# Kernel tuning notes

Measured on AMD Instinct MI355X. Metric: run time of the kernel, lower is better.

## Reference

```python
import jax, jax.numpy as jnp
import numpy as np

GRID = 96  # grid_size from __init__


def setup_inputs() -> dict:
    key = jax.random.key(0)
    k1, k2 = jax.random.split(key)
    B, N, D = 8, 4096, 128
    node_features = jax.random.normal(k1, (N, D), dtype=jnp.float32)
    # pixel coordinates in [0, GRID)
    node_positions = jax.random.uniform(k2, (N, 2), dtype=jnp.float32) * GRID
    # sorted batch assignment with equal node counts per sample
    batch_idx = jnp.repeat(jnp.arange(B, dtype=jnp.int32), N // B)
    log_sigma = jnp.log(jnp.float32(4.0))  # learnable parameter, init sigma=4.0
    return {
        "node_features": node_features,
        "node_positions": node_positions,
        "batch_idx": batch_idx,
        "batch_size": B,
        "log_sigma": log_sigma,
    }


def reference(node_features, node_positions, batch_idx, batch_size, log_sigma):
    # node_features: (N, D); node_positions: (N, 2); batch_idx: (N,) sorted,
    # equal counts per sample (so grouping is a reshape).
    N, D = node_features.shape
    G = GRID
    coords = jnp.arange(G, dtype=jnp.float32)  # shared y and x coords
    dy = coords[None, :] - node_positions[:, 0:1]  # (N, G)
    dx = coords[None, :] - node_positions[:, 1:2]  # (N, G)
    # per-node distance map over the grid, matching torch's sqrt-then-square
    dist = jnp.sqrt(dy[:, :, None] ** 2 + dx[:, None, :] ** 2)  # (N, G, G)
    sigma = jnp.exp(log_sigma)
    w = jnp.exp(-(dist ** 2) / (2.0 * sigma ** 2)).reshape(N, G * G)
    w = w / (jnp.sum(w, axis=1, keepdims=True) + 1e-8)  # normalized splat weights
    n_per = N // batch_size
    f = node_features.reshape(batch_size, n_per, D)
    wB = w.reshape(batch_size, n_per, G * G)
    # grid[b, d, p] = sum_n f[b, n, d] * w[b, n, p]  (scatter-splat accumulation)
    grid = jnp.einsum('bnd,bnp->bdp', f, wB)
    return grid.reshape(batch_size, D, G, G)
```

## Files before the change

### kernel.cpp

```cpp
#include <hip/hip_runtime.h>
#include <hip/hip_bf16.h>

#define GG    96
#define DD    128
#define KC    32
#define APAD  40
#define RCUT  18
#define NWIN  18
#define NPER  512

typedef __attribute__((ext_vector_type(8))) short short8v;
typedef __attribute__((ext_vector_type(4))) float f32x4;

__global__ __launch_bounds__(256, 3) void splat_all(
    const float* __restrict__ f, const float* __restrict__ pos,
    const float* __restrict__ log_sigma, float* __restrict__ out,
    int Nn, int n_per)
{
    const int swz = ((int)blockIdx.x % 8) * GG + (int)blockIdx.x / 8;
    const int b = swz / GG;
    const int y = swz % GG;
    const int tid = (int)threadIdx.x;
    const int lane = tid & 63;
    const int wvid = tid >> 6;
    const int lr = lane & 15;
    const int kg = lane >> 4;
    const int kpw = tid & 15;
    const int nbase = b * NPER;
    const float yf = (float)y;

    __shared__ int ghist[8][GG];
    __shared__ int gpart[8][GG];
    __shared__ int spre[GG + 1];
    __shared__ int inv[NPER];
    __shared__ int wtot;
    __shared__ float spy_s[NPER], spx_s[NPER], sg_s[NPER];
    __shared__ float tSy[NPER], tSx[NPER];
    __shared__ __align__(16) unsigned short sW[2][GG][APAD];

    for (int i = tid; i < 8 * GG; i += 256) (&ghist[0][0])[i] = 0;
    __syncthreads();

    int binA, binB;
    {
        float pyA = pos[(size_t)(nbase + tid) * 2];
        float pyB = pos[(size_t)(nbase + tid + 256) * 2];
        binA = (int)floorf(pyA); binA = binA < 0 ? 0 : (binA > GG - 1 ? GG - 1 : binA);
        binB = (int)floorf(pyB); binB = binB < 0 ? 0 : (binB > GG - 1 ? GG - 1 : binB);
        atomicAdd(&ghist[wvid][binA], 1);
        atomicAdd(&ghist[4 + wvid][binB], 1);
    }
    const unsigned long long below = (lane == 0) ? 0ull : (~0ull >> (64 - lane));
    unsigned long long mA = ~0ull, mB = ~0ull;
#pragma unroll
    for (int bit = 0; bit < 7; ++bit) {
        unsigned long long bA = __ballot((binA >> bit) & 1);
        unsigned long long bB = __ballot((binB >> bit) & 1);
        mA &= ((binA >> bit) & 1) ? bA : ~bA;
        mB &= ((binB >> bit) & 1) ? bB : ~bB;
    }
    const int rA = __popcll(mA & below);
    const int rB = __popcll(mB & below);
    __syncthreads();

    int bc = 0;
    if (tid < GG) {
        int s = 0;
#pragma unroll
        for (int g = 0; g < 8; ++g) { gpart[g][tid] = s; s += ghist[g][tid]; }
        bc = s;
    }
    int xs = bc;
#pragma unroll
    for (int off = 1; off < 64; off <<= 1) {
        int v = __shfl_up(xs, off, 64);
        if (lane >= off) xs += v;
    }
    if (tid == 63) wtot = xs;
    __syncthreads();
    if (tid >= 64 && tid < GG) xs += wtot;
    if (tid < GG) spre[tid + 1] = xs;
    if (tid == 0) spre[0] = 0;
    __syncthreads();

    inv[spre[binA] + gpart[wvid][binA] + rA]     = tid;
    inv[spre[binB] + gpart[4 + wvid][binB] + rB] = tid + 256;
    __syncthreads();

    const int lob = y - RCUT < 0 ? 0 : y - RCUT;
    const int hib = y + RCUT > GG ? GG : y + RCUT;
    const int klo = spre[lob];
    const int khi = spre[hib];
    const int c0 = klo >> 5;
    const int c1 = (khi + 31) >> 5;
    const int jlo = c0 * KC, jhi = c1 * KC;
    const int nb = jhi - jlo;

    for (int i = tid; i < nb; i += 256) {
        int j = jlo + i, nl = inv[j];
        spy_s[j] = pos[(size_t)(nbase + nl) * 2 + 0];
        spx_s[j] = pos[(size_t)(nbase + nl) * 2 + 1];
    }
    __syncthreads();

    const float sig = expf(log_sigma[0]);
    const float inv2s2 = 1.0f / (2.0f * sig * sig);

    for (int i = tid; i < 2 * nb; i += 256) {
        int j = jlo + (i >> 1);
        float p = (i & 1) ? spx_s[j] : spy_s[j];
        int fp = (int)floorf(p);
        int w0 = fp - (NWIN - 1); if (w0 < 0) w0 = 0;
        int w1 = fp + NWIN;       if (w1 > GG - 1) w1 = GG - 1;
        float s = 0.f;
        for (int yy = w0; yy <= w1; ++yy) {
            float d = (float)yy - p;
            s += __expf(-d * d * inv2s2);
        }
        if (i & 1) tSx[j] = s; else tSy[j] = s;
    }
    __syncthreads();
    for (int i = tid; i < nb; i += 256) {
        int j = jlo + i;
        sg_s[j] = 1.0f / (tSy[j] * tSx[j] + 1e-8f);
    }
    __syncthreads();

    f32x4 acc[2][6];
#pragma unroll
    for (int mi = 0; mi < 2; ++mi)
#pragma unroll
        for (int ni = 0; ni < 6; ++ni) acc[mi][ni] = (f32x4){0.f, 0.f, 0.f, 0.f};

    const int ar0 = wvid * 32 + lr;
    const float* fcol = f + (size_t)nbase * DD + ar0;

#define WGEN(CC, BUF)                                                              \
    {                                                                              \
        const int j0_ = (CC) * KC + 2 * kpw;                                       \
        const float py0_ = spy_s[j0_], py1_ = spy_s[j0_ + 1];                      \
        const float px0_ = spx_s[j0_], px1_ = spx_s[j0_ + 1];                      \
        const float g0_ = sg_s[j0_],  g1_ = sg_s[j0_ + 1];                         \
        const float dy0_ = yf - py0_, dy1_ = yf - py1_;                            \
        const float ey0_ = __expf(-dy0_ * dy0_ * inv2s2) * g0_;                    \
        const float ey1_ = __expf(-dy1_ * dy1_ * inv2s2) * g1_;                    \
        _Pragma("unroll")                                                          \
        for (int i_ = 0; i_ < 6; ++i_) {                                           \
            int x_  = (tid + 256 * i_) >> 4;                                       \
            float xf_ = (float)x_;                                                 \
            float dx0_ = xf_ - px0_, dx1_ = xf_ - px1_;                            \
            float w0_ = ey0_ * __expf(-dx0_ * dx0_ * inv2s2);                      \
            float w1_ = ey1_ * __expf(-dx1_ * dx1_ * inv2s2);                      \
            __hip_bfloat162 bb_ = __float22bfloat162_rn(make_float2(w0_, w1_));    \
            *(unsigned int*)&sW[BUF][x_][2 * kpw] = *(unsigned int*)&bb_;          \
        }                                                                          \
    }

#define PKPAIR(X0, X1, HI, LO)                                                     \
    {                                                                              \
        __hip_bfloat162 h_ = __float22bfloat162_rn(make_float2((X0), (X1)));       \
        unsigned int hu_; __builtin_memcpy(&hu_, &h_, 4);                          \
        unsigned int b0_ = hu_ << 16, b1_ = hu_ & 0xFFFF0000u;                     \
        float h0_, h1_;                                                            \
        __builtin_memcpy(&h0_, &b0_, 4);                                           \
        __builtin_memcpy(&h1_, &b1_, 4);                                           \
        __hip_bfloat162 l_ = __float22bfloat162_rn(                                \
            make_float2((X0) - h0_, (X1) - h1_));                                  \
        (HI) = hu_; __builtin_memcpy(&(LO), &l_, 4);                               \
    }

    if (c0 < c1) WGEN(c0, 0);
    __syncthreads();

    int cur = 0;
    for (int c = c0; c < c1; ++c) {
        int4 iv0 = *(const int4*)&inv[c * KC + kg * 8];
        int4 iv1 = *(const int4*)&inv[c * KC + kg * 8 + 4];
        float v00 = fcol[(size_t)iv0.x * DD],      v01 = fcol[(size_t)iv0.y * DD];
        float v02 = fcol[(size_t)iv0.z * DD],      v03 = fcol[(size_t)iv0.w * DD];
        float v04 = fcol[(size_t)iv1.x * DD],      v05 = fcol[(size_t)iv1.y * DD];
        float v06 = fcol[(size_t)iv1.z * DD],      v07 = fcol[(size_t)iv1.w * DD];
        float v10 = fcol[(size_t)iv0.x * DD + 16], v11 = fcol[(size_t)iv0.y * DD + 16];
        float v12 = fcol[(size_t)iv0.z * DD + 16], v13 = fcol[(size_t)iv0.w * DD + 16];
        float v14 = fcol[(size_t)iv1.x * DD + 16], v15 = fcol[(size_t)iv1.y * DD + 16];
        float v16 = fcol[(size_t)iv1.z * DD + 16], v17 = fcol[(size_t)iv1.w * DD + 16];

        if (c + 1 < c1) WGEN(c + 1, cur ^ 1);

        union U { unsigned int u[4]; short8v v; } H0, L0, H1, L1;
        PKPAIR(v00, v01, H0.u[0], L0.u[0]);
        PKPAIR(v02, v03, H0.u[1], L0.u[1]);
        PKPAIR(v04, v05, H0.u[2], L0.u[2]);
        PKPAIR(v06, v07, H0.u[3], L0.u[3]);
        PKPAIR(v10, v11, H1.u[0], L1.u[0]);
        PKPAIR(v12, v13, H1.u[1], L1.u[1]);
        PKPAIR(v14, v15, H1.u[2], L1.u[2]);
        PKPAIR(v16, v17, H1.u[3], L1.u[3]);
        short8v cah0 = H0.v, cal0 = L0.v, cah1 = H1.v, cal1 = L1.v;

#pragma unroll
        for (int ni = 0; ni < 6; ++ni) {
            short8v bv = *(const short8v*)&sW[cur][ni * 16 + lr][kg * 8];
            acc[0][ni] = __builtin_amdgcn_mfma_f32_16x16x32_bf16(cah0, bv, acc[0][ni], 0, 0, 0);
            acc[1][ni] = __builtin_amdgcn_mfma_f32_16x16x32_bf16(cah1, bv, acc[1][ni], 0, 0, 0);
            acc[0][ni] = __builtin_amdgcn_mfma_f32_16x16x32_bf16(cal0, bv, acc[0][ni], 0, 0, 0);
            acc[1][ni] = __builtin_amdgcn_mfma_f32_16x16x32_bf16(cal1, bv, acc[1][ni], 0, 0, 0);
        }
        __syncthreads();
        cur ^= 1;
    }

#pragma unroll
    for (int mi = 0; mi < 2; ++mi)
#pragma unroll
        for (int ni = 0; ni < 6; ++ni) {
            const int d0 = wvid * 32 + mi * 16 + kg * 4;
            const int x  = ni * 16 + lr;
            float* op = out + (((size_t)b * DD + d0) * GG + y) * GG + x;
#pragma unroll
            for (int r = 0; r < 4; ++r)
                __builtin_nontemporal_store(acc[mi][ni][r], op + (size_t)r * GG * GG);
        }
#undef WGEN
#undef PKPAIR
}

extern "C" void kernel_launch(void* const* d_in, const int* in_sizes, int n_in,
                              void* d_out, int out_size, void* d_ws, size_t ws_size,
                              hipStream_t stream) {
    const float* feat = (const float*)d_in[0];
    const float* pos  = (const float*)d_in[1];
    const float* lsig = (const float*)d_in[4];

    const int N  = in_sizes[2];
    const int B  = out_size / (DD * GG * GG);
    const int n_per = N / B;

    splat_all<<<B * GG, 256, 0, stream>>>(feat, pos, lsig, (float*)d_out, N, n_per);
}
```

Before: 26.25 us.

## Drop bf16 low-part split of features and tighten chunk window alignment

Features were split into bf16 high and low parts with two MFMAs each. Now only the high part is kept, which halves the MFMA count and removes the residual packing work. The node-window chunking also starts at the exact first needed node instead of a 32-aligned boundary, clamped to the end of the sample, so fewer chunks are processed per row. Dropping the low part lowers feature precision to plain bf16, which risks accuracy-tolerance failures.

```diff
diff --git a/kernel.cpp b/kernel.cpp
--- a/kernel.cpp
+++ b/kernel.cpp
@@ -91,13 +91,13 @@
     const int hib = y + RCUT > GG ? GG : y + RCUT;
     const int klo = spre[lob];
     const int khi = spre[hib];
-    const int c0 = klo >> 5;
-    const int c1 = (khi + 31) >> 5;
-    const int jlo = c0 * KC, jhi = c1 * KC;
-    const int nb = jhi - jlo;
-
-    for (int i = tid; i < nb; i += 256) {
-        int j = jlo + i, nl = inv[j];
+    const int nch = (khi - klo + KC - 1) >> 5;
+    int j0 = klo;
+    if (j0 + nch * KC > NPER) j0 = NPER - nch * KC;
+    const int nbw = nch * KC;
+
+    for (int i = tid; i < nbw; i += 256) {
+        int j = j0 + i, nl = inv[j];
         spy_s[j] = pos[(size_t)(nbase + nl) * 2 + 0];
         spx_s[j] = pos[(size_t)(nbase + nl) * 2 + 1];
     }
@@ -106,8 +106,8 @@
     const float sig = expf(log_sigma[0]);
     const float inv2s2 = 1.0f / (2.0f * sig * sig);
 
-    for (int i = tid; i < 2 * nb; i += 256) {
-        int j = jlo + (i >> 1);
+    for (int i = tid; i < 2 * nbw; i += 256) {
+        int j = j0 + (i >> 1);
         float p = (i & 1) ? spx_s[j] : spy_s[j];
         int fp = (int)floorf(p);
         int w0 = fp - (NWIN - 1); if (w0 < 0) w0 = 0;
@@ -120,8 +120,8 @@
         if (i & 1) tSx[j] = s; else tSy[j] = s;
     }
     __syncthreads();
-    for (int i = tid; i < nb; i += 256) {
-        int j = jlo + i;
+    for (int i = tid; i < nbw; i += 256) {
+        int j = j0 + i;
         sg_s[j] = 1.0f / (tSy[j] * tSx[j] + 1e-8f);
     }
     __syncthreads();
@@ -137,7 +137,7 @@
 
 #define WGEN(CC, BUF)                                                              \
     {                                                                              \
-        const int j0_ = (CC) * KC + 2 * kpw;                                       \
+        const int j0_ = j0 + (CC) * KC + 2 * kpw;                                  \
         const float py0_ = spy_s[j0_], py1_ = spy_s[j0_ + 1];                      \
         const float px0_ = spx_s[j0_], px1_ = spx_s[j0_ + 1];                      \
         const float g0_ = sg_s[j0_],  g1_ = sg_s[j0_ + 1];                         \
@@ -156,26 +156,19 @@
         }                                                                          \
     }
 
-#define PKPAIR(X0, X1, HI, LO)                                                     \
+#define PKHI(X0, X1, HI)                                                           \
     {                                                                              \
         __hip_bfloat162 h_ = __float22bfloat162_rn(make_float2((X0), (X1)));       \
-        unsigned int hu_; __builtin_memcpy(&hu_, &h_, 4);                          \
-        unsigned int b0_ = hu_ << 16, b1_ = hu_ & 0xFFFF0000u;                     \
-        float h0_, h1_;                                                            \
-        __builtin_memcpy(&h0_, &b0_, 4);                                           \
-        __builtin_memcpy(&h1_, &b1_, 4);                                           \
-        __hip_bfloat162 l_ = __float22bfloat162_rn(                                \
-            make_float2((X0) - h0_, (X1) - h1_));                                  \
-        (HI) = hu_; __builtin_memcpy(&(LO), &l_, 4);                               \
-    }
-
-    if (c0 < c1) WGEN(c0, 0);
+        __builtin_memcpy(&(HI), &h_, 4);                                           \
+    }
+
+    if (nch > 0) WGEN(0, 0);
     __syncthreads();
 
     int cur = 0;
-    for (int c = c0; c < c1; ++c) {
-        int4 iv0 = *(const int4*)&inv[c * KC + kg * 8];
-        int4 iv1 = *(const int4*)&inv[c * KC + kg * 8 + 4];
+    for (int c = 0; c < nch; ++c) {
+        int4 iv0 = *(const int4*)&inv[j0 + c * KC + kg * 8];
+        int4 iv1 = *(const int4*)&inv[j0 + c * KC + kg * 8 + 4];
         float v00 = fcol[(size_t)iv0.x * DD],      v01 = fcol[(size_t)iv0.y * DD];
         float v02 = fcol[(size_t)iv0.z * DD],      v03 = fcol[(size_t)iv0.w * DD];
         float v04 = fcol[(size_t)iv1.x * DD],      v05 = fcol[(size_t)iv1.y * DD];
@@ -185,26 +178,24 @@
         float v14 = fcol[(size_t)iv1.x * DD + 16], v15 = fcol[(size_t)iv1.y * DD + 16];
         float v16 = fcol[(size_t)iv1.z * DD + 16], v17 = fcol[(size_t)iv1.w * DD + 16];
 
-        if (c + 1 < c1) WGEN(c + 1, cur ^ 1);
-
-        union U { unsigned int u[4]; short8v v; } H0, L0, H1, L1;
-        PKPAIR(v00, v01, H0.u[0], L0.u[0]);
-        PKPAIR(v02, v03, H0.u[1], L0.u[1]);
-        PKPAIR(v04, v05, H0.u[2], L0.u[2]);
-        PKPAIR(v06, v07, H0.u[3], L0.u[3]);
-        PKPAIR(v10, v11, H1.u[0], L1.u[0]);
-        PKPAIR(v12, v13, H1.u[1], L1.u[1]);
-        PKPAIR(v14, v15, H1.u[2], L1.u[2]);
-        PKPAIR(v16, v17, H1.u[3], L1.u[3]);
-        short8v cah0 = H0.v, cal0 = L0.v, cah1 = H1.v, cal1 = L1.v;
+        if (c + 1 < nch) WGEN(c + 1, cur ^ 1);
+
+        union U { unsigned int u[4]; short8v v; } H0, H1;
+        PKHI(v00, v01, H0.u[0]);
+        PKHI(v02, v03, H0.u[1]);
+        PKHI(v04, v05, H0.u[2]);
+        PKHI(v06, v07, H0.u[3]);
+        PKHI(v10, v11, H1.u[0]);
+        PKHI(v12, v13, H1.u[1]);
+        PKHI(v14, v15, H1.u[2]);
+        PKHI(v16, v17, H1.u[3]);
+        short8v cah0 = H0.v, cah1 = H1.v;
 
 #pragma unroll
         for (int ni = 0; ni < 6; ++ni) {
             short8v bv = *(const short8v*)&sW[cur][ni * 16 + lr][kg * 8];
             acc[0][ni] = __builtin_amdgcn_mfma_f32_16x16x32_bf16(cah0, bv, acc[0][ni], 0, 0, 0);
             acc[1][ni] = __builtin_amdgcn_mfma_f32_16x16x32_bf16(cah1, bv, acc[1][ni], 0, 0, 0);
-            acc[0][ni] = __builtin_amdgcn_mfma_f32_16x16x32_bf16(cal0, bv, acc[0][ni], 0, 0, 0);
-            acc[1][ni] = __builtin_amdgcn_mfma_f32_16x16x32_bf16(cal1, bv, acc[1][ni], 0, 0, 0);
         }
         __syncthreads();
         cur ^= 1;
@@ -222,7 +213,7 @@
                 __builtin_nontemporal_store(acc[mi][ni][r], op + (size_t)r * GG * GG);
         }
 #undef WGEN
-#undef PKPAIR
+#undef PKHI
 }
 
 extern "C" void kernel_launch(void* const* d_in, const int* in_sizes, int n_in,
```

New measurement: 23.84 us. -9.2%, faster.
